# Kernel tuning notes

Measured on AMD Instinct MI355X. Metric: run time of the kernel, lower is better.

## Reference

```python
import jax, jax.numpy as jnp
import numpy as np

N_NODES = 50000
N_EDGES = 800000
DIM_IN = 128
DIM_OUT = 64


def setup_inputs() -> dict:
    key = jax.random.key(0)
    k1, k2, k3, k4 = jax.random.split(key, 4)
    x = jax.random.normal(k1, (N_NODES, DIM_IN), dtype=jnp.float32)
    edge_index = jax.random.randint(k2, (2, N_EDGES), 0, N_NODES, dtype=jnp.int64)
    W = jax.random.normal(k3, (DIM_IN, DIM_OUT), dtype=jnp.float32) / np.sqrt(DIM_IN)
    b = jax.random.normal(k4, (DIM_OUT,), dtype=jnp.float32) * 0.01
    return {"x": x, "edge_index": edge_index, "W": W, "b": b}


def reference(x, edge_index, W, b):
    # Faithful PyG GCNConv: add self-loops, symmetric deg normalization,
    # linear transform then normalized scatter-add aggregation, then bias.
    N = x.shape[0]
    h = x @ W  # [N, dim_out] — transform before propagate (PyG order)

    loops = jnp.arange(N, dtype=edge_index.dtype)
    src = jnp.concatenate([edge_index[0], loops])  # [E+N]
    dst = jnp.concatenate([edge_index[1], loops])  # [E+N]

    ones = jnp.ones(src.shape[0], dtype=h.dtype)
    deg = jax.ops.segment_sum(ones, dst, num_segments=N)  # in-degree incl. self-loop
    dinv = jnp.where(deg > 0, jax.lax.rsqrt(deg), 0.0)
    norm = dinv[src] * dinv[dst]  # [E+N]

    msgs = h[src] * norm[:, None]  # gather + scale
    out = jax.ops.segment_sum(msgs, dst, num_segments=N) + b  # scatter-add
    return jax.nn.log_softmax(out, axis=1)
```

## Files before the change

### kernel.cpp

```cpp
#include <hip/hip_runtime.h>
#include <hip/hip_fp16.h>
#include <cstdint>
#include <cstddef>

#define N_NODES 50000
#define N_EDGES 800000
#define DIM_IN  128
#define DIM_OUT 64

#define BSHIFT  5
#define BNODES  32
#define NB      2048
#define NBK     ((N_NODES + BNODES - 1) / BNODES)
#define EB      4096
#define SORTB   ((N_EDGES + EB - 1) / EB)
#define NE4     (N_EDGES / 4)
#define GROWS   128

typedef _Float16 f16x8 __attribute__((ext_vector_type(8)));
typedef float    f32x4 __attribute__((ext_vector_type(4)));

__global__ __launch_bounds__(256) void kA_hist(const int* __restrict__ ei,
                                               int* __restrict__ M) {
    __shared__ int hcnt[NB];
    const int t = threadIdx.x, blk = blockIdx.x;
    for (int i = t; i < NB; i += 256) hcnt[i] = 0;
    __syncthreads();
    const int4* dst4 = (const int4*)(ei + N_EDGES);
#pragma unroll
    for (int it = 0; it < EB / 1024; ++it) {
        const int g = blk * (EB / 4) + it * 256 + t;
        if (g < NE4) {
            const int4 d = dst4[g];
            atomicAdd(&hcnt[d.x >> BSHIFT], 1);
            atomicAdd(&hcnt[d.y >> BSHIFT], 1);
            atomicAdd(&hcnt[d.z >> BSHIFT], 1);
            atomicAdd(&hcnt[d.w >> BSHIFT], 1);
        }
    }
    __syncthreads();
    for (int i = t; i < NB; i += 256) M[blk * NB + i] = hcnt[i];
}

__global__ __launch_bounds__(256) void kB_tile(const int* __restrict__ M,
                                               int* __restrict__ startsL,
                                               int* __restrict__ colsum) {
    __shared__ int s[256];
    const int b = blockIdx.x, t = threadIdx.x;
    const int v = (t < SORTB) ? M[(size_t)t * NB + b] : 0;
    s[t] = v;
    __syncthreads();
    for (int off = 1; off < 256; off <<= 1) {
        int add = (t >= off) ? s[t - off] : 0;
        __syncthreads();
        s[t] += add;
        __syncthreads();
    }
    if (t < SORTB) startsL[(size_t)t * NB + b] = s[t] - v;
    if (t == 255) colsum[b] = s[255];
}

__global__ __launch_bounds__(1024) void kB_scan(const int* __restrict__ colsum,
                                                int* __restrict__ bstart) {
    __shared__ int s[1024];
    const int t = threadIdx.x;
    const int2 v2 = ((const int2*)colsum)[t];
    const int pair = v2.x + v2.y;
    s[t] = pair;
    __syncthreads();
    for (int off = 1; off < 1024; off <<= 1) {
        int add = (t >= off) ? s[t - off] : 0;
        __syncthreads();
        s[t] += add;
        __syncthreads();
    }
    const int excl = s[t] - pair;
    bstart[2 * t]     = excl;
    bstart[2 * t + 1] = excl + v2.x;
    if (t == 1023) bstart[NB] = s[1023];
}

__global__ __launch_bounds__(256) void kC_scatter(const int* __restrict__ ei,
                                                  const int* __restrict__ startsL,
                                                  const int* __restrict__ bstart,
                                                  unsigned* __restrict__ pairs) {
    __shared__ int cur[NB];
    const int t = threadIdx.x, blk = blockIdx.x;
    for (int i = t; i < NB; i += 256)
        cur[i] = bstart[i] + startsL[(size_t)blk * NB + i];
    __syncthreads();
    const int4* src4 = (const int4*)ei;
    const int4* dst4 = (const int4*)(ei + N_EDGES);
#pragma unroll
    for (int it = 0; it < EB / 1024; ++it) {
        const int g = blk * (EB / 4) + it * 256 + t;
        if (g < NE4) {
            const int4 sv = src4[g];
            const int4 dv = dst4[g];
            int p;
            p = atomicAdd(&cur[dv.x >> BSHIFT], 1); pairs[p] = ((unsigned)sv.x << 16) | (unsigned)dv.x;
            p = atomicAdd(&cur[dv.y >> BSHIFT], 1); pairs[p] = ((unsigned)sv.y << 16) | (unsigned)dv.y;
            p = atomicAdd(&cur[dv.z >> BSHIFT], 1); pairs[p] = ((unsigned)sv.z << 16) | (unsigned)dv.z;
            p = atomicAdd(&cur[dv.w >> BSHIFT], 1); pairs[p] = ((unsigned)sv.w << 16) | (unsigned)dv.w;
        }
    }
}

__global__ __launch_bounds__(256) void kSort(const unsigned* __restrict__ pairs,
                                             const int* __restrict__ bstart,
                                             unsigned short* __restrict__ csr,
                                             int* __restrict__ nodeoff,
                                             float* __restrict__ dinv) {
    __shared__ int cnt[BNODES];
    __shared__ int cur[BNODES];
    const int b = blockIdx.x, t = threadIdx.x;
    const int eb = bstart[b], ee = bstart[b + 1];

    if (t < BNODES) cnt[t] = 0;
    __syncthreads();

    for (int i = eb + t; i < ee; i += 256)
        atomicAdd(&cnt[pairs[i] & (BNODES - 1)], 1);
    __syncthreads();

    if (t < 64) {
        const int lane = t;
        const int v = (lane < BNODES) ? cnt[lane] : 0;
        int xs = v;
#pragma unroll
        for (int off = 1; off < BNODES; off <<= 1) {
            int y = __shfl_up(xs, off);
            if (lane >= off) xs += y;
        }
        if (lane < BNODES) {
            const int excl = xs - v;
            cur[lane] = eb + excl;
            const int n = (b << BSHIFT) + lane;
            if (n <= N_NODES) nodeoff[n] = eb + excl;
            if (n < N_NODES)  dinv[n] = rsqrtf((float)(v + 1));
        }
    }
    __syncthreads();

    for (int i = eb + t; i < ee; i += 256) {
        const unsigned p = pairs[i];
        const int pos = atomicAdd(&cur[p & (BNODES - 1)], 1);
        csr[pos] = (unsigned short)(p >> 16);
    }
}

__global__ __launch_bounds__(256) void k_gemm(const float* __restrict__ x,
                                              const float* __restrict__ W,
                                              const float* __restrict__ dinv,
                                              __half* __restrict__ h) {
    const int t = threadIdx.x;
    const int w = t >> 6;
    const int l = t & 63;
    const int q = l >> 4;
    const int m16 = l & 15;

    f16x8 bf[4][4];
#pragma unroll
    for (int kc = 0; kc < 4; ++kc)
#pragma unroll
        for (int ct = 0; ct < 4; ++ct) {
            const float* wp = W + (size_t)(kc * 32 + q * 8) * DIM_OUT + ct * 16 + m16;
            f16x8 v;
#pragma unroll
            for (int j = 0; j < 8; ++j) v[j] = (_Float16)wp[(size_t)j * DIM_OUT];
            bf[kc][ct] = v;
        }

    const int base = blockIdx.x * GROWS + w * 32;
#pragma unroll
    for (int rt = 0; rt < 2; ++rt) {
        const int m0 = base + rt * 16;
        int mrow = m0 + m16;
        if (mrow >= N_NODES) mrow = N_NODES - 1;

        f16x8 af[4];
#pragma unroll
        for (int kc = 0; kc < 4; ++kc) {
            const float4* xp = (const float4*)(x + (size_t)mrow * DIM_IN + kc * 32 + q * 8);
            const float4 p0 = xp[0], p1 = xp[1];
            f16x8 a;
            a[0] = (_Float16)p0.x; a[1] = (_Float16)p0.y;
            a[2] = (_Float16)p0.z; a[3] = (_Float16)p0.w;
            a[4] = (_Float16)p1.x; a[5] = (_Float16)p1.y;
            a[6] = (_Float16)p1.z; a[7] = (_Float16)p1.w;
            af[kc] = a;
        }

        f32x4 acc[4];
#pragma unroll
        for (int ct = 0; ct < 4; ++ct) acc[ct] = (f32x4){0.f, 0.f, 0.f, 0.f};
#pragma unroll
        for (int kc = 0; kc < 4; ++kc)
#pragma unroll
            for (int ct = 0; ct < 4; ++ct)
                acc[ct] = __builtin_amdgcn_mfma_f32_16x16x32_f16(af[kc], bf[kc][ct], acc[ct], 0, 0, 0);

#pragma unroll
        for (int reg = 0; reg < 4; ++reg) {
            const int r = m0 + q * 4 + reg;
            if (r < N_NODES) {
                const float d = dinv[r];
#pragma unroll
                for (int ct = 0; ct < 4; ++ct)
                    h[(size_t)r * DIM_OUT + ct * 16 + m16] = __float2half(acc[ct][reg] * d);
            }
        }
    }
}

__global__ __launch_bounds__(256) void kE_agg(const int* __restrict__ nodeoff,
                                              const unsigned short* __restrict__ csr,
                                              const __half* __restrict__ h,
                                              const float* __restrict__ bvec,
                                              float* __restrict__ out) {
    const int t = threadIdx.x;
    const int hw = t >> 5, sl = t & 31;
    const int n = blockIdx.x * 8 + hw;
    const __half2* __restrict__ h2 = (const __half2*)h;

    const int s0 = nodeoff[n], s1 = nodeoff[n + 1];
    float2 acc = __half22float2(h2[n * 32 + sl]);

    int i = s0;
    for (; i + 4 <= s1; i += 4) {
        const int a0 = csr[i + 0];
        const int a1 = csr[i + 1];
        const int a2 = csr[i + 2];
        const int a3 = csr[i + 3];
        const float2 v0 = __half22float2(h2[a0 * 32 + sl]);
        const float2 v1 = __half22float2(h2[a1 * 32 + sl]);
        const float2 v2 = __half22float2(h2[a2 * 32 + sl]);
        const float2 v3 = __half22float2(h2[a3 * 32 + sl]);
        acc.x += v0.x + v1.x + v2.x + v3.x;
        acc.y += v0.y + v1.y + v2.y + v3.y;
    }
    for (; i < s1; ++i) {
        const float2 v0 = __half22float2(h2[csr[i] * 32 + sl]);
        acc.x += v0.x; acc.y += v0.y;
    }

    const float2 bias = *(const float2*)&bvec[2 * sl];
    const float di = rsqrtf((float)(s1 - s0 + 1));
    float vx = acc.x * di + bias.x;
    float vy = acc.y * di + bias.y;

    float m = fmaxf(vx, vy);
#pragma unroll
    for (int off = 16; off > 0; off >>= 1) m = fmaxf(m, __shfl_xor(m, off));
    float s = __expf(vx - m) + __expf(vy - m);
#pragma unroll
    for (int off = 16; off > 0; off >>= 1) s += __shfl_xor(s, off);
    const float ls = __logf(s);

    float2 o; o.x = vx - m - ls; o.y = vy - m - ls;
    *(float2*)&out[(size_t)n * DIM_OUT + 2 * sl] = o;
}

extern "C" void kernel_launch(void* const* d_in, const int* in_sizes, int n_in,
                              void* d_out, int out_size, void* d_ws, size_t ws_size,
                              hipStream_t stream) {
    const float* x  = (const float*)d_in[0];
    const int*   ei = (const int*)d_in[1];
    const float* W  = (const float*)d_in[2];
    const float* b  = (const float*)d_in[3];
    float* out = (float*)d_out;

    char* ws = (char*)d_ws;
    __half*         h       = (__half*)ws;         ws += (size_t)N_NODES * DIM_OUT * sizeof(__half);
    float*          dinv    = (float*)ws;          ws += (size_t)N_NODES * sizeof(float);
    unsigned*       pairs   = (unsigned*)ws;       ws += (size_t)N_EDGES * sizeof(unsigned);
    unsigned short* csr     = (unsigned short*)ws; ws += (size_t)N_EDGES * sizeof(unsigned short);
    int*            nodeoff = (int*)ws;            ws += (size_t)(N_NODES + 1) * sizeof(int);
    ws = (char*)(((uintptr_t)ws + 15) & ~(uintptr_t)15);
    int*            M       = (int*)ws;            ws += (size_t)SORTB * NB * sizeof(int);
    int*            startsL = (int*)ws;            ws += (size_t)SORTB * NB * sizeof(int);
    int*            colsum  = (int*)ws;            ws += (size_t)NB * sizeof(int);
    int*            bstart  = (int*)ws;            ws += (size_t)(NB + 1) * sizeof(int);

    kA_hist   <<<SORTB, 256, 0, stream>>>(ei, M);
    kB_tile   <<<NB, 256, 0, stream>>>(M, startsL, colsum);
    kB_scan   <<<1, 1024, 0, stream>>>(colsum, bstart);
    kC_scatter<<<SORTB, 256, 0, stream>>>(ei, startsL, bstart, pairs);
    kSort     <<<NBK, 256, 0, stream>>>(pairs, bstart, csr, nodeoff, dinv);
    k_gemm    <<<(N_NODES + GROWS - 1) / GROWS, 256, 0, stream>>>(x, W, dinv, h);
    kE_agg    <<<N_NODES / 8, 256, 0, stream>>>(nodeoff, csr, h, b, out);
}
```

Before: 138.6 us.

## Widen aggregation gathers to 8-byte loads and batch edges per sort block

The aggregation kernel now assigns 16 lanes per node, each gathering four halves with one 8-byte load instead of two halves per lane, and runs 16 nodes per block. The sort kernel's count and placement loops are unrolled four-wide so several pair loads are in flight before the shared atomics. The edge-block size for the histogram and scatter passes doubles, halving the number of sort blocks and the size of the per-block histogram matrix. The wider gathers cut instruction count per neighbour but leave fewer lanes per node row, and larger edge blocks reduce parallelism in the early passes.

```diff
diff --git a/kernel.cpp b/kernel.cpp
--- a/kernel.cpp
+++ b/kernel.cpp
@@ -12,12 +12,13 @@
 #define BNODES  32
 #define NB      2048
 #define NBK     ((N_NODES + BNODES - 1) / BNODES)
-#define EB      4096
+#define EB      8192
 #define SORTB   ((N_EDGES + EB - 1) / EB)
 #define NE4     (N_EDGES / 4)
 #define GROWS   128
 
 typedef _Float16 f16x8 __attribute__((ext_vector_type(8)));
+typedef _Float16 f16x4 __attribute__((ext_vector_type(4)));
 typedef float    f32x4 __attribute__((ext_vector_type(4)));
 
 __global__ __launch_bounds__(256) void kA_hist(const int* __restrict__ ei,
@@ -119,8 +120,20 @@
     if (t < BNODES) cnt[t] = 0;
     __syncthreads();
 
-    for (int i = eb + t; i < ee; i += 256)
-        atomicAdd(&cnt[pairs[i] & (BNODES - 1)], 1);
+    {
+        int i = eb + t;
+        for (; i + 768 < ee; i += 1024) {
+            const unsigned p0 = pairs[i];
+            const unsigned p1 = pairs[i + 256];
+            const unsigned p2 = pairs[i + 512];
+            const unsigned p3 = pairs[i + 768];
+            atomicAdd(&cnt[p0 & (BNODES - 1)], 1);
+            atomicAdd(&cnt[p1 & (BNODES - 1)], 1);
+            atomicAdd(&cnt[p2 & (BNODES - 1)], 1);
+            atomicAdd(&cnt[p3 & (BNODES - 1)], 1);
+        }
+        for (; i < ee; i += 256) atomicAdd(&cnt[pairs[i] & (BNODES - 1)], 1);
+    }
     __syncthreads();
 
     if (t < 64) {
@@ -142,10 +155,24 @@
     }
     __syncthreads();
 
-    for (int i = eb + t; i < ee; i += 256) {
-        const unsigned p = pairs[i];
-        const int pos = atomicAdd(&cur[p & (BNODES - 1)], 1);
-        csr[pos] = (unsigned short)(p >> 16);
+    {
+        int i = eb + t;
+        for (; i + 768 < ee; i += 1024) {
+            const unsigned p0 = pairs[i];
+            const unsigned p1 = pairs[i + 256];
+            const unsigned p2 = pairs[i + 512];
+            const unsigned p3 = pairs[i + 768];
+            int q;
+            q = atomicAdd(&cur[p0 & (BNODES - 1)], 1); csr[q] = (unsigned short)(p0 >> 16);
+            q = atomicAdd(&cur[p1 & (BNODES - 1)], 1); csr[q] = (unsigned short)(p1 >> 16);
+            q = atomicAdd(&cur[p2 & (BNODES - 1)], 1); csr[q] = (unsigned short)(p2 >> 16);
+            q = atomicAdd(&cur[p3 & (BNODES - 1)], 1); csr[q] = (unsigned short)(p3 >> 16);
+        }
+        for (; i < ee; i += 256) {
+            const unsigned p = pairs[i];
+            const int q = atomicAdd(&cur[p & (BNODES - 1)], 1);
+            csr[q] = (unsigned short)(p >> 16);
+        }
     }
 }
 
@@ -219,46 +246,53 @@
                                               const float* __restrict__ bvec,
                                               float* __restrict__ out) {
     const int t = threadIdx.x;
-    const int hw = t >> 5, sl = t & 31;
-    const int n = blockIdx.x * 8 + hw;
-    const __half2* __restrict__ h2 = (const __half2*)h;
+    const int qw = t >> 4, sl = t & 15;
+    const int n = blockIdx.x * 16 + qw;
+    const f16x4* __restrict__ h4 = (const f16x4*)h;
 
     const int s0 = nodeoff[n], s1 = nodeoff[n + 1];
-    float2 acc = __half22float2(h2[n * 32 + sl]);
+
+    const f16x4 hv = h4[n * 16 + sl];
+    float a0f = (float)hv[0], a1f = (float)hv[1], a2f = (float)hv[2], a3f = (float)hv[3];
 
     int i = s0;
     for (; i + 4 <= s1; i += 4) {
-        const int a0 = csr[i + 0];
-        const int a1 = csr[i + 1];
-        const int a2 = csr[i + 2];
-        const int a3 = csr[i + 3];
-        const float2 v0 = __half22float2(h2[a0 * 32 + sl]);
-        const float2 v1 = __half22float2(h2[a1 * 32 + sl]);
-        const float2 v2 = __half22float2(h2[a2 * 32 + sl]);
-        const float2 v3 = __half22float2(h2[a3 * 32 + sl]);
-        acc.x += v0.x + v1.x + v2.x + v3.x;
-        acc.y += v0.y + v1.y + v2.y + v3.y;
+        const int c0 = csr[i + 0];
+        const int c1 = csr[i + 1];
+        const int c2 = csr[i + 2];
+        const int c3 = csr[i + 3];
+        const f16x4 v0 = h4[c0 * 16 + sl];
+        const f16x4 v1 = h4[c1 * 16 + sl];
+        const f16x4 v2 = h4[c2 * 16 + sl];
+        const f16x4 v3 = h4[c3 * 16 + sl];
+        a0f += (float)v0[0] + (float)v1[0] + (float)v2[0] + (float)v3[0];
+        a1f += (float)v0[1] + (float)v1[1] + (float)v2[1] + (float)v3[1];
+        a2f += (float)v0[2] + (float)v1[2] + (float)v2[2] + (float)v3[2];
+        a3f += (float)v0[3] + (float)v1[3] + (float)v2[3] + (float)v3[3];
     }
     for (; i < s1; ++i) {
-        const float2 v0 = __half22float2(h2[csr[i] * 32 + sl]);
-        acc.x += v0.x; acc.y += v0.y;
-    }
-
-    const float2 bias = *(const float2*)&bvec[2 * sl];
+        const f16x4 v0 = h4[csr[i] * 16 + sl];
+        a0f += (float)v0[0]; a1f += (float)v0[1]; a2f += (float)v0[2]; a3f += (float)v0[3];
+    }
+
+    const float4 bias = *(const float4*)&bvec[4 * sl];
     const float di = rsqrtf((float)(s1 - s0 + 1));
-    float vx = acc.x * di + bias.x;
-    float vy = acc.y * di + bias.y;
-
-    float m = fmaxf(vx, vy);
-#pragma unroll
-    for (int off = 16; off > 0; off >>= 1) m = fmaxf(m, __shfl_xor(m, off));
-    float s = __expf(vx - m) + __expf(vy - m);
-#pragma unroll
-    for (int off = 16; off > 0; off >>= 1) s += __shfl_xor(s, off);
+    float v0 = a0f * di + bias.x;
+    float v1 = a1f * di + bias.y;
+    float v2 = a2f * di + bias.z;
+    float v3 = a3f * di + bias.w;
+
+    float m = fmaxf(fmaxf(v0, v1), fmaxf(v2, v3));
+#pragma unroll
+    for (int off = 8; off > 0; off >>= 1) m = fmaxf(m, __shfl_xor(m, off));
+    float s = __expf(v0 - m) + __expf(v1 - m) + __expf(v2 - m) + __expf(v3 - m);
+#pragma unroll
+    for (int off = 8; off > 0; off >>= 1) s += __shfl_xor(s, off);
     const float ls = __logf(s);
 
-    float2 o; o.x = vx - m - ls; o.y = vy - m - ls;
-    *(float2*)&out[(size_t)n * DIM_OUT + 2 * sl] = o;
+    float4 o;
+    o.x = v0 - m - ls; o.y = v1 - m - ls; o.z = v2 - m - ls; o.w = v3 - m - ls;
+    *(float4*)&out[(size_t)n * DIM_OUT + 4 * sl] = o;
 }
 
 extern "C" void kernel_launch(void* const* d_in, const int* in_sizes, int n_in,
@@ -288,5 +322,5 @@
     kC_scatter<<<SORTB, 256, 0, stream>>>(ei, startsL, bstart, pairs);
     kSort     <<<NBK, 256, 0, stream>>>(pairs, bstart, csr, nodeoff, dinv);
     k_gemm    <<<(N_NODES + GROWS - 1) / GROWS, 256, 0, stream>>>(x, W, dinv, h);
-    kE_agg    <<<N_NODES / 8, 256, 0, stream>>>(nodeoff, csr, h, b, out);
-}
+    kE_agg    <<<N_NODES / 16, 256, 0, stream>>>(nodeoff, csr, h, b, out);
+}
```

Result: faster. 131.9 us (-4.8%).
